# Kernel tuning notes

Hardware: AMD Instinct MI355X
Metric: run time of the kernel (lower is better)

The kernel has to match this reference:

```python
import jax, jax.numpy as jnp
import numpy as np

B, D_IN, UNITS = 8192, 4096, 4096

def setup_inputs() -> dict:
    key = jax.random.key(0)
    k1, k2 = jax.random.split(key)
    x = jax.random.normal(k1, (B, D_IN), dtype=jnp.float32)
    kernel = jax.random.normal(k2, (D_IN, UNITS), dtype=jnp.float32) * 0.02  # glorot-ish scale
    bias = jnp.zeros((UNITS,), dtype=jnp.float32)
    return {"x": x, "kernel": kernel, "bias": bias}

def reference(x, kernel, bias):
    # BinaryDense: binarize weights via sign, then dense matmul + bias
    kernel_bin = jnp.sign(kernel)                     # [D_IN, UNITS], values in {-1,0,+1}
    out = jnp.matmul(x, kernel_bin) + bias            # [B, UNITS]
    return out
```

## Files before the change

### kernel.cpp

```cpp
#include <hip/hip_runtime.h>
#include <stdint.h>


typedef int int4v __attribute__((ext_vector_type(4)));
typedef int int16v __attribute__((ext_vector_type(16)));

constexpr int M = 8192, N = 4096, K = 4096;
constexpr int BM = 256, BN = 256, BK = 64;
constexpr int NT = K / BK;

__device__ __forceinline__ void gload_lds16(const void* g, void* l) {
  __builtin_amdgcn_global_load_lds(
      (const __attribute__((address_space(1))) unsigned int*)g,
      (__attribute__((address_space(3))) unsigned int*)l, 16, 0, 0);
}

#define FENCE asm volatile("" ::: "memory")

__global__ __launch_bounds__(256) void prep_kernel(const float* __restrict__ x,
                                                   signed char* __restrict__ xq,
                                                   float* __restrict__ rscale,
                                                   const float* __restrict__ w,
                                                   signed char* __restrict__ wq) {
  const int t = threadIdx.x;
  if (blockIdx.x < M) {
    const int row = blockIdx.x;
    const float* xr = x + (size_t)row * K;
    float4 v[4];
    float mx = 0.f;
#pragma unroll
    for (int i = 0; i < 4; ++i) {
      v[i] = *(const float4*)(xr + t * 16 + i * 4);
      mx = fmaxf(mx, fmaxf(fmaxf(fabsf(v[i].x), fabsf(v[i].y)),
                           fmaxf(fabsf(v[i].z), fabsf(v[i].w))));
    }
#pragma unroll
    for (int off = 32; off >= 1; off >>= 1)
      mx = fmaxf(mx, __shfl_xor(mx, off, 64));
    __shared__ float smax[4];
    if ((t & 63) == 0) smax[t >> 6] = mx;
    __syncthreads();
    const float rm = fmaxf(fmaxf(smax[0], smax[1]), fmaxf(smax[2], smax[3]));
    const float s = (rm > 0.f) ? 127.f / rm : 0.f;
    if (t == 0) rscale[row] = (rm > 0.f) ? rm / 127.f : 0.f;
    uint32_t o[4];
#pragma unroll
    for (int i = 0; i < 4; ++i) {
      float f[4] = {v[i].x, v[i].y, v[i].z, v[i].w};
      uint32_t p = 0;
#pragma unroll
      for (int j = 0; j < 4; ++j) {
        int q = (int)rintf(f[j] * s);
        p |= ((uint32_t)(uint8_t)(signed char)q) << (8 * j);
      }
      o[i] = p;
    }
    *(int4v*)(xq + (size_t)row * K + t * 16) =
        (int4v){(int)o[0], (int)o[1], (int)o[2], (int)o[3]};
  } else {
    __shared__ __align__(16) signed char tile[64 * 68];
    const int idx = blockIdx.x - M;
    const int n0 = (idx & 63) * 64, k0 = (idx >> 6) * 64;
#pragma unroll
    for (int i = 0; i < 4; ++i) {
      int kl = (t >> 4) + i * 16;
      int nl = (t & 15) * 4;
      float4 v = *(const float4*)(w + (size_t)(k0 + kl) * N + n0 + nl);
      uint32_t p = 0;
      p |= ((uint32_t)(uint8_t)(signed char)((v.x > 0.f) - (v.x < 0.f)));
      p |= ((uint32_t)(uint8_t)(signed char)((v.y > 0.f) - (v.y < 0.f))) << 8;
      p |= ((uint32_t)(uint8_t)(signed char)((v.z > 0.f) - (v.z < 0.f))) << 16;
      p |= ((uint32_t)(uint8_t)(signed char)((v.w > 0.f) - (v.w < 0.f))) << 24;
      *(uint32_t*)(tile + kl * 68 + nl) = p;
    }
    __syncthreads();
    const int nl = t >> 2;
    const int kc = (t & 3) * 16;
    uint32_t o[4] = {0, 0, 0, 0};
#pragma unroll
    for (int j = 0; j < 16; ++j)
      o[j >> 2] |= ((uint32_t)(uint8_t)tile[(kc + j) * 68 + nl]) << (8 * (j & 3));
    *(int4v*)(wq + (size_t)(n0 + nl) * K + k0 + kc) =
        (int4v){(int)o[0], (int)o[1], (int)o[2], (int)o[3]};
  }
}


#define RD_SET(AN, BN_, P, KK)                                                 \
  {                                                                            \
    _Pragma("unroll") for (int mi_ = 0; mi_ < 4; ++mi_) {                      \
      const int r_ = wm * 128 + mi_ * 32 + l31;                                \
      const int sl_ = ((KK)*2 + hi) ^ ((r_ >> 1) & 3);                         \
      AN[mi_] = *(const int4v*)(smem + (P)*32768 + r_ * 64 + sl_ * 16);        \
    }                                                                          \
    _Pragma("unroll") for (int ni_ = 0; ni_ < 2; ++ni_) {                      \
      const int r_ = wn * 64 + ni_ * 32 + l31;                                 \
      const int sl_ = ((KK)*2 + hi) ^ ((r_ >> 1) & 3);                         \
      BN_[ni_] = *(const int4v*)(smem + (P)*32768 + 16384 + r_ * 64 +          \
                                 sl_ * 16);                                    \
    }                                                                          \
  }

#define MM(AN, BN_)                                                            \
  {                                                                            \
    __builtin_amdgcn_s_setprio(1);                                             \
    _Pragma("unroll") for (int mi_ = 0; mi_ < 4; ++mi_) {                      \
      _Pragma("unroll") for (int ni_ = 0; ni_ < 2; ++ni_) {                    \
        acc[mi_][ni_] = __builtin_amdgcn_mfma_i32_32x32x32_i8(                 \
            AN[mi_], BN_[ni_], acc[mi_][ni_], 0, 0, 0);                        \
      }                                                                        \
    }                                                                          \
    __builtin_amdgcn_s_setprio(0);                                             \
  }

#define TILE(P, Q, S, T)                                                       \
  {                                                                            \
    RD_SET(aY, bY, P, 1);                                                      \
    const bool more2_ = (T) + 2 < NT;                                          \
    if (more2_) stage(S, (T) + 2);                                             \
    MM(aX, bX);                                                                \
    if (more2_) {                                                              \
      asm volatile("s_waitcnt vmcnt(4)" ::: "memory");                         \
    } else {                                                                   \
      asm volatile("s_waitcnt vmcnt(0)" ::: "memory");                         \
    }                                                                          \
    __builtin_amdgcn_s_barrier();                                              \
    FENCE;                                                                     \
    if ((T) + 1 < NT) RD_SET(aX, bX, Q, 0);                                    \
    MM(aY, bY);                                                                \
    FENCE;                                                                     \
  }

__global__ __launch_bounds__(512, 2) void gemm_bin_kernel(
    const signed char* __restrict__ Xq,
    const signed char* __restrict__ Wq,
    const float* __restrict__ rscale,
    const float* __restrict__ bias,
    float* __restrict__ out) {
  __shared__ __align__(16) signed char smem[131072];

  const int tid = threadIdx.x;
  const int w = tid >> 6;
  const int lane = tid & 63;
  const int wm = w >> 2;
  const int wn = w & 3;
  const int hi = lane >> 5;
  const int l31 = lane & 31;
  const size_t m0 = (size_t)blockIdx.y * BM;
  const size_t n0 = (size_t)blockIdx.x * BN;

  int16v acc[4][2];
#pragma unroll
  for (int i = 0; i < 4; ++i)
#pragma unroll
    for (int j = 0; j < 2; ++j)
#pragma unroll
      for (int r = 0; r < 16; ++r) acc[i][j][r] = 0;
  int4v aX[4], bX[2], aY[4], bY[2];

  auto stage = [&](int pb, int t) {
    signed char* lb = smem + pb * 32768;
#pragma unroll
    for (int it = 0; it < 2; ++it) {
      int pos = it * 512 + tid;
      int row = pos >> 2, s = pos & 3;
      int qg = s ^ ((row >> 1) & 3);
      gload_lds16(Xq + (m0 + row) * (size_t)K + (size_t)t * BK + qg * 16,
                  lb + pos * 16);
    }
#pragma unroll
    for (int it = 0; it < 2; ++it) {
      int pos = it * 512 + tid;
      int row = pos >> 2, s = pos & 3;
      int qg = s ^ ((row >> 1) & 3);
      gload_lds16(Wq + (n0 + row) * (size_t)K + (size_t)t * BK + qg * 16,
                  lb + 16384 + pos * 16);
    }
  };

  stage(0, 0);
  stage(1, 1);
  asm volatile("s_waitcnt vmcnt(4)" ::: "memory");
  __builtin_amdgcn_s_barrier();
  FENCE;
  RD_SET(aX, bX, 0, 0);

#pragma unroll 1
  for (int t = 0; t < NT; t += 4) {
    TILE(0, 1, 2, t)
    TILE(1, 2, 3, t + 1)
    TILE(2, 3, 0, t + 2)
    TILE(3, 0, 1, t + 3)
  }

#pragma unroll
  for (int mi = 0; mi < 4; ++mi) {
    const size_t rbase = m0 + wm * 128 + mi * 32;
    float sc[4][4];
#pragma unroll
    for (int q = 0; q < 4; ++q)
      *(float4*)sc[q] = *(const float4*)(rscale + rbase + hi * 4 + q * 8);
#pragma unroll
    for (int ni = 0; ni < 2; ++ni) {
      const size_t col = n0 + wn * 64 + ni * 32 + l31;
      const float bv = bias[col];
#pragma unroll
      for (int r = 0; r < 16; ++r) {
        const int row = (r & 3) + 8 * (r >> 2) + 4 * hi;
        out[(rbase + row) * N + col] = (float)acc[mi][ni][r] * sc[r >> 2][r & 3] + bv;
      }
    }
  }
}

extern "C" void kernel_launch(void* const* d_in, const int* in_sizes, int n_in,
                              void* d_out, int out_size, void* d_ws, size_t ws_size,
                              hipStream_t stream) {
  const float* x = (const float*)d_in[0];
  const float* kern = (const float*)d_in[1];
  const float* bias = (const float*)d_in[2];
  float* out = (float*)d_out;

  signed char* Xq = (signed char*)d_ws;
  signed char* Wq = Xq + (size_t)M * K;
  float* rscale = (float*)(Wq + (size_t)N * K);

  prep_kernel<<<M + (N / 64) * (K / 64), 256, 0, stream>>>(x, Xq, rscale, kern, Wq);
  gemm_bin_kernel<<<dim3(N / BN, M / BM), 512, 0, stream>>>(Xq, Wq, rscale, bias, out);
}
```

Baseline: 392.5 us.

## Pre-swizzle quantized operands into MFMA-fragment band layout for contiguous loads

Both quantized operands are rearranged in global memory into 32-row bands, where each 64-wide K tile is stored as four 16-byte chunks per row grouped in MFMA fragment order. The X rearrangement happens in place in a second prep kernel, and W is written straight into this layout. The GEMM's global-to-LDS loads and LDS fragment reads then become plain linear offsets (lane*16) without XOR swizzling. The goal is simpler address arithmetic and conflict-free LDS reads. The cost is an extra kernel launch plus another full read and write pass over Xq, and reads within a band rely on the in-place permute being race-free.

New measurement: 395.3 us. About the same (+0.7%).

```diff
diff --git a/kernel.cpp b/kernel.cpp
--- a/kernel.cpp
+++ b/kernel.cpp
@@ -8,6 +8,7 @@
 constexpr int M = 8192, N = 4096, K = 4096;
 constexpr int BM = 256, BN = 256, BK = 64;
 constexpr int NT = K / BK;
+constexpr int BANDSZ = 131072;
 
 __device__ __forceinline__ void gload_lds16(const void* g, void* l) {
   __builtin_amdgcn_global_load_lds(
@@ -17,49 +18,51 @@
 
 #define FENCE asm volatile("" ::: "memory")
 
-__global__ __launch_bounds__(256) void prep_kernel(const float* __restrict__ x,
-                                                   signed char* __restrict__ xq,
-                                                   float* __restrict__ rscale,
-                                                   const float* __restrict__ w,
-                                                   signed char* __restrict__ wq) {
+__global__ __launch_bounds__(256) void quant_x_kernel(const float* __restrict__ x,
+                                                      signed char* __restrict__ xq,
+                                                      float* __restrict__ rscale) {
+  const int row = blockIdx.x;
   const int t = threadIdx.x;
-  if (blockIdx.x < M) {
-    const int row = blockIdx.x;
-    const float* xr = x + (size_t)row * K;
-    float4 v[4];
-    float mx = 0.f;
-#pragma unroll
-    for (int i = 0; i < 4; ++i) {
-      v[i] = *(const float4*)(xr + t * 16 + i * 4);
-      mx = fmaxf(mx, fmaxf(fmaxf(fabsf(v[i].x), fabsf(v[i].y)),
-                           fmaxf(fabsf(v[i].z), fabsf(v[i].w))));
-    }
-#pragma unroll
-    for (int off = 32; off >= 1; off >>= 1)
-      mx = fmaxf(mx, __shfl_xor(mx, off, 64));
-    __shared__ float smax[4];
-    if ((t & 63) == 0) smax[t >> 6] = mx;
-    __syncthreads();
-    const float rm = fmaxf(fmaxf(smax[0], smax[1]), fmaxf(smax[2], smax[3]));
-    const float s = (rm > 0.f) ? 127.f / rm : 0.f;
-    if (t == 0) rscale[row] = (rm > 0.f) ? rm / 127.f : 0.f;
-    uint32_t o[4];
-#pragma unroll
-    for (int i = 0; i < 4; ++i) {
-      float f[4] = {v[i].x, v[i].y, v[i].z, v[i].w};
-      uint32_t p = 0;
-#pragma unroll
-      for (int j = 0; j < 4; ++j) {
-        int q = (int)rintf(f[j] * s);
-        p |= ((uint32_t)(uint8_t)(signed char)q) << (8 * j);
-      }
-      o[i] = p;
-    }
-    *(int4v*)(xq + (size_t)row * K + t * 16) =
-        (int4v){(int)o[0], (int)o[1], (int)o[2], (int)o[3]};
-  } else {
+  const float* xr = x + (size_t)row * K;
+  float4 v[4];
+  float mx = 0.f;
+#pragma unroll
+  for (int i = 0; i < 4; ++i) {
+    v[i] = *(const float4*)(xr + t * 16 + i * 4);
+    mx = fmaxf(mx, fmaxf(fmaxf(fabsf(v[i].x), fabsf(v[i].y)),
+                         fmaxf(fabsf(v[i].z), fabsf(v[i].w))));
+  }
+#pragma unroll
+  for (int off = 32; off >= 1; off >>= 1)
+    mx = fmaxf(mx, __shfl_xor(mx, off, 64));
+  __shared__ float smax[4];
+  if ((t & 63) == 0) smax[t >> 6] = mx;
+  __syncthreads();
+  const float rm = fmaxf(fmaxf(smax[0], smax[1]), fmaxf(smax[2], smax[3]));
+  const float s = (rm > 0.f) ? 127.f / rm : 0.f;
+  if (t == 0) rscale[row] = (rm > 0.f) ? rm / 127.f : 0.f;
+  uint32_t o[4];
+#pragma unroll
+  for (int i = 0; i < 4; ++i) {
+    float f[4] = {v[i].x, v[i].y, v[i].z, v[i].w};
+    uint32_t p = 0;
+#pragma unroll
+    for (int j = 0; j < 4; ++j) {
+      int q = (int)rintf(f[j] * s);
+      p |= ((uint32_t)(uint8_t)(signed char)q) << (8 * j);
+    }
+    o[i] = p;
+  }
+  *(int4v*)(xq + (size_t)row * K + t * 16) = (int4v){(int)o[0], (int)o[1], (int)o[2], (int)o[3]};
+}
+
+__global__ __launch_bounds__(256) void prep2_kernel(const float* __restrict__ w,
+                                                    signed char* __restrict__ wq,
+                                                    signed char* __restrict__ xq) {
+  const int t = threadIdx.x;
+  if (blockIdx.x < 4096) {
     __shared__ __align__(16) signed char tile[64 * 68];
-    const int idx = blockIdx.x - M;
+    const int idx = blockIdx.x;
     const int n0 = (idx & 63) * 64, k0 = (idx >> 6) * 64;
 #pragma unroll
     for (int i = 0; i < 4; ++i) {
@@ -75,13 +78,32 @@
     }
     __syncthreads();
     const int nl = t >> 2;
-    const int kc = (t & 3) * 16;
+    const int ci = t & 3;
     uint32_t o[4] = {0, 0, 0, 0};
 #pragma unroll
     for (int j = 0; j < 16; ++j)
-      o[j >> 2] |= ((uint32_t)(uint8_t)tile[(kc + j) * 68 + nl]) << (8 * (j & 3));
-    *(int4v*)(wq + (size_t)(n0 + nl) * K + k0 + kc) =
+      o[j >> 2] |= ((uint32_t)(uint8_t)tile[(ci * 16 + j) * 68 + nl]) << (8 * (j & 3));
+    const int n = n0 + nl;
+    const int nband = n >> 5, n31 = n & 31;
+    const int tt = k0 >> 6;
+    *(int4v*)(wq + (size_t)nband * BANDSZ + tt * 2048 + ci * 512 + n31 * 16) =
         (int4v){(int)o[0], (int)o[1], (int)o[2], (int)o[3]};
+  } else {
+    const int band = blockIdx.x - 4096;
+    signed char* base = xq + (size_t)band * BANDSZ;
+    const int r31 = t & 31, cp = t >> 5;
+    int4v v[32];
+#pragma unroll
+    for (int g = 0; g < 32; ++g) {
+      const int idx = g * 8 + cp;
+      v[g] = *(const int4v*)(base + r31 * 4096 + (idx >> 2) * 64 + (idx & 3) * 16);
+    }
+    __syncthreads();
+#pragma unroll
+    for (int g = 0; g < 32; ++g) {
+      const int idx = g * 8 + cp;
+      *(int4v*)(base + idx * 512 + r31 * 16) = v[g];
+    }
   }
 }
 
@@ -89,15 +111,12 @@
 #define RD_SET(AN, BN_, P, KK)                                                 \
   {                                                                            \
     _Pragma("unroll") for (int mi_ = 0; mi_ < 4; ++mi_) {                      \
-      const int r_ = wm * 128 + mi_ * 32 + l31;                                \
-      const int sl_ = ((KK)*2 + hi) ^ ((r_ >> 1) & 3);                         \
-      AN[mi_] = *(const int4v*)(smem + (P)*32768 + r_ * 64 + sl_ * 16);        \
+      AN[mi_] = *(const int4v*)(smem + (P)*32768 + wm * 8192 + mi_ * 2048 +    \
+                                (KK)*1024 + lane16);                           \
     }                                                                          \
     _Pragma("unroll") for (int ni_ = 0; ni_ < 2; ++ni_) {                      \
-      const int r_ = wn * 64 + ni_ * 32 + l31;                                 \
-      const int sl_ = ((KK)*2 + hi) ^ ((r_ >> 1) & 3);                         \
-      BN_[ni_] = *(const int4v*)(smem + (P)*32768 + 16384 + r_ * 64 +          \
-                                 sl_ * 16);                                    \
+      BN_[ni_] = *(const int4v*)(smem + (P)*32768 + 16384 + wn * 4096 +        \
+                                 ni_ * 2048 + (KK)*1024 + lane16);             \
     }                                                                          \
   }
 
@@ -146,6 +165,7 @@
   const int wn = w & 3;
   const int hi = lane >> 5;
   const int l31 = lane & 31;
+  const int lane16 = lane * 16;
   const size_t m0 = (size_t)blockIdx.y * BM;
   const size_t n0 = (size_t)blockIdx.x * BN;
 
@@ -158,22 +178,24 @@
       for (int r = 0; r < 16; ++r) acc[i][j][r] = 0;
   int4v aX[4], bX[2], aY[4], bY[2];
 
+  const size_t abase0 = (m0 >> 5) * (size_t)BANDSZ;
+  const size_t bbase0 = (n0 >> 5) * (size_t)BANDSZ;
   auto stage = [&](int pb, int t) {
     signed char* lb = smem + pb * 32768;
+    const size_t at = abase0 + (size_t)t * 2048;
+    const size_t bt = bbase0 + (size_t)t * 2048;
 #pragma unroll
     for (int it = 0; it < 2; ++it) {
       int pos = it * 512 + tid;
-      int row = pos >> 2, s = pos & 3;
-      int qg = s ^ ((row >> 1) & 3);
-      gload_lds16(Xq + (m0 + row) * (size_t)K + (size_t)t * BK + qg * 16,
+      gload_lds16(Xq + at + (size_t)(pos >> 7) * BANDSZ + ((pos >> 6) & 1) * 1024 +
+                      (pos & 63) * 16,
                   lb + pos * 16);
     }
 #pragma unroll
     for (int it = 0; it < 2; ++it) {
       int pos = it * 512 + tid;
-      int row = pos >> 2, s = pos & 3;
-      int qg = s ^ ((row >> 1) & 3);
-      gload_lds16(Wq + (n0 + row) * (size_t)K + (size_t)t * BK + qg * 16,
+      gload_lds16(Wq + bt + (size_t)(pos >> 7) * BANDSZ + ((pos >> 6) & 1) * 1024 +
+                      (pos & 63) * 16,
                   lb + 16384 + pos * 16);
     }
   };
@@ -225,6 +247,7 @@
   signed char* Wq = Xq + (size_t)M * K;
   float* rscale = (float*)(Wq + (size_t)N * K);
 
-  prep_kernel<<<M + (N / 64) * (K / 64), 256, 0, stream>>>(x, Xq, rscale, kern, Wq);
+  quant_x_kernel<<<M, 256, 0, stream>>>(x, Xq, rscale);
+  prep2_kernel<<<4096 + 256, 256, 0, stream>>>(kern, Wq, Xq);
   gemm_bin_kernel<<<dim3(N / BN, M / BM), 512, 0, stream>>>(Xq, Wq, rscale, bias, out);
 }
```
